# Optimization experiments

Hardware: AMD Instinct MI355X
Metric: run time of the kernel (lower is better)

The kernel has to match this reference:

```python
import jax, jax.numpy as jnp
import numpy as np
import math

RES = 1024          # FastTrigLookup / FastPhaseProcessor resolution
TWO_PI = 2.0 * math.pi
D = 512             # model dim


def setup_inputs() -> dict:
    key = jax.random.key(0)
    ks = jax.random.split(key, 4)
    B, L = 4, 4096

    def xavier(k, shape):
        fan_out, fan_in = shape
        std = math.sqrt(2.0 / (fan_in + fan_out))
        return jax.random.normal(k, shape, jnp.float32) * std

    return {
        "x": jax.random.normal(ks[0], (B, L, D), jnp.float32),
        "ft_w": xavier(ks[1], (2 * D, D)),
        "ft_b": jnp.zeros((2 * D,), jnp.float32),
        "ln_g": jnp.ones((2 * D,), jnp.float32),
        "ln_b": jnp.zeros((2 * D,), jnp.float32),
        "exc": jnp.ones((1,), jnp.float32) * 0.1,  # excitation_factor init
        "qkv_w": xavier(ks[2], (6 * D, 6 * D)),
        "qkv_b": jnp.zeros((6 * D,), jnp.float32),
        "op_w": xavier(ks[3], (2 * D, 2 * D)),
        "op_b": jnp.zeros((2 * D,), jnp.float32),
    }


def _forward(x, ft_w, ft_b, ln_g, ln_b, exc, qkv_w, qkv_b, op_w, op_b):
    B, L = x.shape[:2]
    sin_tab = jnp.sin(jnp.linspace(0.0, TWO_PI, RES)).astype(x.dtype)
    cos_tab = jnp.cos(jnp.linspace(0.0, TWO_PI, RES)).astype(x.dtype)

    # --- SimpleQuantumState: fused Linear -> tanh-GELU -> LayerNorm ---
    t = x @ ft_w.T + ft_b                                  # [B,L,2D]
    c1, c2 = 0.044715, math.sqrt(2.0 / math.pi)
    g = 0.5 * t * (1.0 + jnp.tanh(c2 * (t + c1 * t ** 3)))
    mu = g.mean(-1, keepdims=True)
    var = ((g - mu) ** 2).mean(-1, keepdims=True)
    n = (g - mu) * jax.lax.rsqrt(var + 1e-5) * ln_g + ln_b
    rp, ip = n[..., :D], n[..., D:]
    # atan2 -> gather-based sin/cos lookup (torch .long() truncates toward 0;
    # negative indices wrap from the end -> emulate with mod RES)
    ang = jnp.arctan2(ip + 1e-8, rp + 1e-8)
    idx = jnp.mod((ang / TWO_PI * (RES - 1)).astype(jnp.int32), RES)
    real = rp * cos_tab[idx]
    imag = ip * sin_tab[idx]
    nrm = jax.lax.rsqrt(real ** 2 + imag ** 2 + 1e-8) * math.sqrt(1.0 / D)
    real, imag = real * nrm, imag * nrm

    # --- EnhancedDynamicPhaseSpace: collapse prevention via trig lookup ---
    amp = jnp.sqrt(real ** 2 + imag ** 2 + 1e-8)
    coll = (amp < 0.1).astype(x.dtype)
    el = jnp.linspace(0.0, 1.0, D) * TWO_PI                # energy_levels * 2pi
    lidx = jnp.clip((jnp.mod(el, TWO_PI) / TWO_PI * RES).astype(jnp.int32), 0, RES - 1)
    real = real + coll * cos_tab[lidx] * exc
    imag = imag + coll * sin_tab[lidx] * exc
    nrm2 = jax.lax.rsqrt(real ** 2 + imag ** 2 + 1e-8)
    real, imag = real * nrm2, imag * nrm2

    # --- BasicQuantumAttention with q=k=v = quantum state (pad_mask=None) ---
    qkv_in = jnp.concatenate([real, imag, real, imag, real, imag], axis=-1)  # [B,L,6D]
    qkv = (qkv_in @ qkv_w.T + qkv_b).reshape(B, L, 6, D)
    q_r, k_r = qkv[:, :, 0], qkv[:, :, 2]
    v_r, v_i = qkv[:, :, 4], qkv[:, :, 5]
    scores = jnp.einsum('bld,bmd->blm', q_r, k_r) * (D ** -0.5)
    attn = jax.nn.softmax(scores, axis=-1)                 # dropout=eval -> identity
    o = jnp.concatenate([jnp.einsum('blm,bmd->bld', attn, v_r),
                         jnp.einsum('blm,bmd->bld', attn, v_i)], axis=-1)
    out = o @ op_w.T + op_b                                # [B,L,2D]
    return out


def reference(x, ft_w, ft_b, ln_g, ln_b, exc, qkv_w, qkv_b, op_w, op_b):
    out = _forward(x, ft_w, ft_b, ln_g, ln_b, exc, qkv_w, qkv_b, op_w, op_b)
    return (out[..., :D], out[..., D:])
```

## Files before the change

### kernel.cpp

```cpp
#include <hip/hip_runtime.h>
#include <hip/hip_bf16.h>
#include <math.h>


#define TWO_PI_F 6.283185307179586f

typedef __attribute__((ext_vector_type(4))) float f32x4;
typedef __attribute__((ext_vector_type(8))) short bf16x8;
typedef __attribute__((ext_vector_type(4))) unsigned short u16x4;
typedef __hip_bfloat16 bf16;

__device__ __forceinline__ void gl_lds16(const void* g, void* l) {
  __builtin_amdgcn_global_load_lds((const __attribute__((address_space(1))) void*)g,
                                   (__attribute__((address_space(3))) void*)l, 16, 0, 0);
}
__device__ __forceinline__ unsigned short f2bf_bits(float f) {
  union { __hip_bfloat16 h; unsigned short u; } cv;
  cv.h = __float2bfloat16(f);
  return cv.u;
}
__device__ __forceinline__ float bf_bits2f(unsigned short b) {
  union { unsigned int u; float f; } cv;
  cv.u = ((unsigned int)b) << 16;
  return cv.f;
}

template <int EPI, int ORD>
__global__ __launch_bounds__(256, 2) void gemm128(
    const bf16* __restrict__ A, const bf16* __restrict__ B, void* __restrict__ C,
    void* __restrict__ Cx, const float* __restrict__ bias, int K, int lda, int ldb, int ldc,
    float scale, long long zsa, long long zsb, long long zsc) {
  __shared__ __align__(16) bf16 sA[128 * 32];
  __shared__ __align__(16) bf16 sB[128 * 32];
  const int tid = threadIdx.x;
  const int lane = tid & 63, wid = tid >> 6;
  const int wm = wid >> 1, wn = wid & 1;

  const int gx = gridDim.x, gy = gridDim.y;
  int flat = blockIdx.x + gx * (blockIdx.y + gy * blockIdx.z);
  {
    const int nwg = gx * gy * gridDim.z;
    const int q = nwg >> 3, r = nwg & 7;
    const int x = flat & 7, loc = flat >> 3;
    flat = (x < r ? x * (q + 1) : r * (q + 1) + (x - r) * q) + loc;
  }
  const int bx = flat % gx;
  const int by = (flat / gx) % gy;
  const int bz = flat / (gx * gy);
  const int bm = by * 128, bn = bx * 128;

  const bf16* Az = A + (long long)bz * zsa;
  const bf16* Bz = B + (long long)bz * zsb;

  f32x4 acc[4][4];
#pragma unroll
  for (int i = 0; i < 4; ++i)
#pragma unroll
    for (int j = 0; j < 4; ++j) acc[i][j] = (f32x4){0.f, 0.f, 0.f, 0.f};

  const int r0 = tid >> 2, r1 = (tid + 256) >> 2, sl = tid & 3;
  const int swzr0 = (r0 & 3) ^ ((r0 >> 2) & 3);
  const int swzr1 = (r1 & 3) ^ ((r1 >> 2) & 3);
  const int ga0 = (sl ^ swzr0) << 3;
  const int ga1 = (sl ^ swzr1) << 3;
  const long long rowA0 = (long long)(bm + r0) * lda;
  const long long rowA1 = (long long)(bm + r1) * lda;
  const long long rowB0 = (long long)(bn + r0) * ldb;
  const long long rowB1 = (long long)(bn + r1) * ldb;

  const int fr = lane & 15, ksl = lane >> 4;

  for (int k0 = 0; k0 < K; k0 += 32) {
    gl_lds16(Az + rowA0 + k0 + ga0, &sA[tid * 8]);
    gl_lds16(Az + rowA1 + k0 + ga1, &sA[(tid + 256) * 8]);
    gl_lds16(Bz + rowB0 + k0 + ga0, &sB[tid * 8]);
    gl_lds16(Bz + rowB1 + k0 + ga1, &sB[(tid + 256) * 8]);
    __syncthreads();
    bf16x8 af[4], bfv[4];
#pragma unroll
    for (int i = 0; i < 4; ++i) {
      const int R = wm * 64 + i * 16 + fr;
      const int s = ksl ^ ((R & 3) ^ ((R >> 2) & 3));
      af[i] = *(const bf16x8*)&sA[R * 32 + s * 8];
    }
#pragma unroll
    for (int j = 0; j < 4; ++j) {
      const int R = wn * 64 + j * 16 + fr;
      const int s = ksl ^ ((R & 3) ^ ((R >> 2) & 3));
      bfv[j] = *(const bf16x8*)&sB[R * 32 + s * 8];
    }
#pragma unroll
    for (int i = 0; i < 4; ++i)
#pragma unroll
      for (int j = 0; j < 4; ++j) {
        if constexpr (ORD == 0)
          acc[i][j] = __builtin_amdgcn_mfma_f32_16x16x32_bf16(af[i], bfv[j], acc[i][j], 0, 0, 0);
        else
          acc[i][j] = __builtin_amdgcn_mfma_f32_16x16x32_bf16(bfv[j], af[i], acc[i][j], 0, 0, 0);
      }
    __syncthreads();
  }

#pragma unroll
  for (int i = 0; i < 4; ++i)
#pragma unroll
    for (int j = 0; j < 4; ++j) {
      if constexpr (ORD == 1) {
        const int row = bm + wm * 64 + i * 16 + fr;
        const int col0 = bn + wn * 64 + j * 16 + ksl * 4;
        f32x4 v = acc[i][j];
#pragma unroll
        for (int r = 0; r < 4; ++r) v[r] *= scale;
        if constexpr (EPI == 0 || EPI == 1) {
          if (bias) {
            const f32x4 bv = *(const f32x4*)&bias[col0];
            v += bv;
          }
        }
        if constexpr (EPI == 1) {
#pragma unroll
          for (int r = 0; r < 4; ++r) {
            const float t = v[r];
            float y = 0.7978845608028654f * (t + 0.044715f * t * t * t);
            y = fminf(fmaxf(y, -15.f), 15.f);
            const float e = __expf(2.f * y);
            v[r] = t * e / (1.f + e);
          }
        }
        if constexpr (EPI == 3) {
          const f32x4 bv = *(const f32x4*)&bias[col0];
          v += bv;
          float* dst = (col0 < 512) ? (float*)C : (float*)Cx;
          const long long rout = zsc + (long long)bz * 4096 + row;
          *(f32x4*)&dst[rout * 512 + (col0 & 511)] = v;
        } else if constexpr (EPI == 2) {
          bf16* cc = (bf16*)C + (long long)bz * zsc;
          u16x4 w;
#pragma unroll
          for (int r = 0; r < 4; ++r) w[r] = f2bf_bits(v[r]);
          *(u16x4*)&cc[(long long)row * ldc + col0] = w;
        } else {
          bf16* cc = (bf16*)C;
          u16x4 w;
#pragma unroll
          for (int r = 0; r < 4; ++r) w[r] = f2bf_bits(v[r]);
          *(u16x4*)&cc[(long long)row * ldc + col0] = w;
        }
      } else {
        const int row0 = bm + wm * 64 + i * 16 + ksl * 4;
        const int d = bn + wn * 64 + j * 16 + fr;
        u16x4 w;
#pragma unroll
        for (int r = 0; r < 4; ++r) w[r] = f2bf_bits(acc[i][j][r] * scale + bias[d]);
        const int b = row0 >> 12, mm = row0 & 4095;
        *(u16x4*)((unsigned short*)Cx + ((long long)(b * 1024 + d)) * 4096 + mm) = w;
      }
    }
  (void)ldc;
}

__global__ __launch_bounds__(256) void ln_phase_kernel(
    const bf16* __restrict__ g, bf16* __restrict__ u, const float* __restrict__ ln_g,
    const float* __restrict__ ln_b, const float* __restrict__ lcos,
    const float* __restrict__ lsin, const float* __restrict__ cost,
    const float* __restrict__ sint) {
  __shared__ float sg[1024];
  __shared__ float red[4];
  const int tid = threadIdx.x;
  const int lane = tid & 63, wid = tid >> 6;
  const long long row = blockIdx.x;
  const bf16* gr = g + row * 1024;

  const u16x4 raw = *(const u16x4*)(gr + tid * 4);
  float lv[4];
  float lsum = 0.f;
#pragma unroll
  for (int e = 0; e < 4; ++e) {
    lv[e] = bf_bits2f(raw[e]);
    lsum += lv[e];
  }
  *(f32x4*)&sg[tid * 4] = *(f32x4*)lv;
#pragma unroll
  for (int off = 32; off > 0; off >>= 1) lsum += __shfl_xor(lsum, off);
  if (lane == 0) red[wid] = lsum;
  __syncthreads();
  const float mu = (red[0] + red[1] + red[2] + red[3]) * (1.0f / 1024.0f);
  __syncthreads();
  float lvar = 0.f;
#pragma unroll
  for (int e = 0; e < 4; ++e) {
    const float d = lv[e] - mu;
    lvar += d * d;
  }
#pragma unroll
  for (int off = 32; off > 0; off >>= 1) lvar += __shfl_xor(lvar, off);
  if (lane == 0) red[wid] = lvar;
  __syncthreads();
  const float var = (red[0] + red[1] + red[2] + red[3]) * (1.0f / 1024.0f);
  const float rs = rsqrtf(var + 1e-5f);

#pragma unroll
  for (int kk = 0; kk < 2; ++kk) {
    const int p = tid + kk * 256;
    const float rp = (sg[p] - mu) * rs * ln_g[p] + ln_b[p];
    const float ip = (sg[p + 512] - mu) * rs * ln_g[p + 512] + ln_b[p + 512];
    const float ang = atan2f(ip + 1e-8f, rp + 1e-8f);
    int idx = (int)((ang / TWO_PI_F) * 1023.0f);
    idx = idx < 0 ? idx + 1024 : idx;
    float real = rp * cost[idx];
    float imag = ip * sint[idx];
    const float nrm = rsqrtf(real * real + imag * imag + 1e-8f) * 0.044194173824159216f;
    real *= nrm;
    imag *= nrm;
    const float amp = sqrtf(real * real + imag * imag + 1e-8f);
    const float coll = (amp < 0.1f) ? 1.0f : 0.0f;
    real += coll * lcos[p];
    imag += coll * lsin[p];
    const float n2 = rsqrtf(real * real + imag * imag + 1e-8f);
    u[row * 1024 + p] = __float2bfloat16(real * n2);
    u[row * 1024 + 512 + p] = __float2bfloat16(imag * n2);
  }
}

__global__ __launch_bounds__(256) void softmax_kernel(bf16* __restrict__ s) {
  __shared__ float ss[4096];
  __shared__ float red[4];
  const int tid = threadIdx.x;
  const int lane = tid & 63, wid = tid >> 6;
  bf16* sr = s + (long long)blockIdx.x * 4096;
  float mx = -3.0e38f;
#pragma unroll
  for (int k = 0; k < 4; ++k) {
    const int base = (k * 256 + tid) * 4;
    const u16x4 raw = *(const u16x4*)(sr + base);
    f32x4 f;
#pragma unroll
    for (int e = 0; e < 4; ++e) {
      f[e] = bf_bits2f(raw[e]);
      mx = fmaxf(mx, f[e]);
    }
    *(f32x4*)&ss[base] = f;
  }
#pragma unroll
  for (int off = 32; off > 0; off >>= 1) mx = fmaxf(mx, __shfl_xor(mx, off));
  if (lane == 0) red[wid] = mx;
  __syncthreads();
  mx = fmaxf(fmaxf(red[0], red[1]), fmaxf(red[2], red[3]));
  __syncthreads();
  float sum = 0.f;
#pragma unroll
  for (int k = 0; k < 4; ++k) {
    const int base = (k * 256 + tid) * 4;
    f32x4 f = *(f32x4*)&ss[base];
#pragma unroll
    for (int e = 0; e < 4; ++e) {
      f[e] = __expf(f[e] - mx);
      sum += f[e];
    }
    *(f32x4*)&ss[base] = f;
  }
#pragma unroll
  for (int off = 32; off > 0; off >>= 1) sum += __shfl_xor(sum, off);
  if (lane == 0) red[wid] = sum;
  __syncthreads();
  const float inv = 1.0f / (red[0] + red[1] + red[2] + red[3]);
#pragma unroll
  for (int k = 0; k < 4; ++k) {
    const int base = (k * 256 + tid) * 4;
    const f32x4 f = *(f32x4*)&ss[base];
    u16x4 w;
#pragma unroll
    for (int e = 0; e < 4; ++e) w[e] = f2bf_bits(f[e] * inv);
    *(u16x4*)(sr + base) = w;
  }
}

__global__ void cast4_f2b(const float* __restrict__ in, bf16* __restrict__ out, long long n4) {
  long long i = (long long)blockIdx.x * blockDim.x + threadIdx.x;
  const long long stride = (long long)gridDim.x * blockDim.x;
  for (; i < n4; i += stride) {
    const f32x4 f = *(const f32x4*)(in + i * 4);
    u16x4 w;
#pragma unroll
    for (int e = 0; e < 4; ++e) w[e] = f2bf_bits(f[e]);
    *(u16x4*)((unsigned short*)out + i * 4) = w;
  }
}

__global__ void fold_qkv(const float* __restrict__ w, const float* __restrict__ b,
                         bf16* __restrict__ weff, float* __restrict__ beff) {
  const int i = blockIdx.x * blockDim.x + threadIdx.x;
  if (i < 1024 * 1024) {
    const int o = i >> 10, j = i & 1023;
    const int so = (o < 512) ? o : o + 512;
    const float* wr = w + (long long)so * 3072;
    weff[i] = __float2bfloat16(wr[j] + wr[1024 + j] + wr[2048 + j]);
    if (j == 0) beff[o] = b[so];
  }
}

__global__ __launch_bounds__(256) void fold_v_t(const float* __restrict__ w,
                                                bf16* __restrict__ wvT) {
  __shared__ float tile[32][33];
  const int t0 = blockIdx.x * 32, j0 = blockIdx.y * 32;
  const int tx = threadIdx.x & 31, ty = threadIdx.x >> 5;
#pragma unroll
  for (int k = 0; k < 4; ++k) {
    const int t = t0 + ty + k * 8;
    const float* wr = w + (long long)(2048 + t) * 3072 + j0 + tx;
    tile[ty + k * 8][tx] = wr[0] + wr[1024] + wr[2048];
  }
  __syncthreads();
#pragma unroll
  for (int k = 0; k < 4; ++k) {
    const int r = ty + k * 8;
    wvT[(long long)(j0 + r) * 1024 + t0 + tx] = __float2bfloat16(tile[tx][r]);
  }
}

__global__ __launch_bounds__(256) void bias_fold2(const float* __restrict__ op_w,
                                                  const float* __restrict__ qkv_b,
                                                  float* __restrict__ beff) {
  __shared__ float red[4];
  const int o = blockIdx.x;
  const int tid = threadIdx.x, lane = tid & 63, wid = tid >> 6;
  float s = 0.f;
#pragma unroll
  for (int k = 0; k < 4; ++k) {
    const int t = tid + k * 256;
    s += op_w[(long long)o * 1024 + t] * qkv_b[2048 + t];
  }
#pragma unroll
  for (int off = 32; off > 0; off >>= 1) s += __shfl_xor(s, off);
  if (lane == 0) red[wid] = s;
  __syncthreads();
  if (tid == 0) beff[1024 + o] = red[0] + red[1] + red[2] + red[3];
}

__global__ void tables_kernel(float* __restrict__ cost, float* __restrict__ sint,
                              float* __restrict__ lcos, float* __restrict__ lsin,
                              const float* __restrict__ exc) {
  const int i = blockIdx.x * blockDim.x + threadIdx.x;
  const double step = 6.283185307179586 / 1023.0;
  if (i < 1024) {
    const float a = (float)((double)i * step);
    cost[i] = cosf(a);
    sint[i] = sinf(a);
  }
  if (i < 512) {
    const float el = ((float)i / 511.0f) * TWO_PI_F;
    const float m = fmodf(el, TWO_PI_F);
    int li = (int)((m / TWO_PI_F) * 1024.0f);
    li = min(max(li, 0), 1023);
    const float a = (float)((double)li * step);
    lcos[i] = cosf(a) * exc[0];
    lsin[i] = sinf(a) * exc[0];
  }
}

extern "C" void kernel_launch(void* const* d_in, const int* in_sizes, int n_in, void* d_out,
                              int out_size, void* d_ws, size_t ws_size, hipStream_t stream) {
  const float* x = (const float*)d_in[0];
  const float* ft_w = (const float*)d_in[1];
  const float* ft_b = (const float*)d_in[2];
  const float* ln_g = (const float*)d_in[3];
  const float* ln_b = (const float*)d_in[4];
  const float* exc = (const float*)d_in[5];
  const float* qkv_w = (const float*)d_in[6];
  const float* qkv_b = (const float*)d_in[7];
  const float* op_w = (const float*)d_in[8];
  const float* op_b = (const float*)d_in[9];

  char* ws = (char*)d_ws;
  const size_t MB = 1024ull * 1024ull;
  bf16* ftw_b = (bf16*)(ws + 0);
  bf16* weff = (bf16*)(ws + 1 * MB);
  bf16* opw_b = (bf16*)(ws + 5 * MB);
  bf16* wvT = (bf16*)(ws + 7 * MB);
  float* beff = (float*)(ws + 9 * MB);
  float* cost = (float*)(ws + 9 * MB + 8192);
  float* sint = (float*)(ws + 9 * MB + 12288);
  float* lcos = (float*)(ws + 9 * MB + 16384);
  float* lsin = (float*)(ws + 9 * MB + 18432);
  bf16* v2T = (bf16*)(ws + 10 * MB);
  bf16* qk = (bf16*)(ws + 42 * MB);
  bf16* x_b = (bf16*)(ws + 74 * MB);
  bf16* gbuf = (bf16*)(ws + 90 * MB);
  bf16* ubuf = (bf16*)(ws + 122 * MB);
  bf16* sc = (bf16*)(ws + 74 * MB);

  cast4_f2b<<<512, 256, 0, stream>>>(ft_w, ftw_b, 131072);
  cast4_f2b<<<1024, 256, 0, stream>>>(op_w, opw_b, 262144);
  cast4_f2b<<<2048, 256, 0, stream>>>(x, x_b, 2097152);
  fold_qkv<<<4096, 256, 0, stream>>>(qkv_w, qkv_b, weff, beff);
  fold_v_t<<<dim3(32, 32), 256, 0, stream>>>(qkv_w, wvT);
  bias_fold2<<<1024, 256, 0, stream>>>(op_w, qkv_b, beff);
  tables_kernel<<<4, 256, 0, stream>>>(cost, sint, lcos, lsin, exc);

  gemm128<0, 1><<<dim3(8, 8), 256, 0, stream>>>(opw_b, wvT, weff + 1024 * 1024, nullptr,
                                                nullptr, 1024, 1024, 1024, 1024, 1.0f, 0, 0, 0);
  gemm128<1, 1><<<dim3(8, 128), 256, 0, stream>>>(x_b, ftw_b, gbuf, nullptr, ft_b, 512, 512,
                                                  512, 1024, 1.0f, 0, 0, 0);
  ln_phase_kernel<<<16384, 256, 0, stream>>>(gbuf, ubuf, ln_g, ln_b, lcos, lsin, cost, sint);
  gemm128<0, 1><<<dim3(8, 128), 256, 0, stream>>>(ubuf, weff, qk, nullptr, beff, 1024, 1024,
                                                  1024, 1024, 1.0f, 0, 0, 0);
  gemm128<4, 0><<<dim3(8, 128), 256, 0, stream>>>(ubuf, weff + 1024 * 1024, nullptr, v2T,
                                                  beff + 1024, 1024, 1024, 1024, 0, 1.0f, 0,
                                                  0, 0);

  float* out0 = (float*)d_out;
  float* out1 = out0 + 8388608LL;
  for (int p = 0; p < 2; ++p) {
    const bf16* qbase = qk + (long long)(2 * p) * 4096 * 1024;
    gemm128<2, 1><<<dim3(32, 32, 2), 256, 0, stream>>>(
        qbase, qbase + 512, sc, nullptr, nullptr, 512, 1024, 1024, 4096,
        0.04419417382415922f, 4096LL * 1024, 4096LL * 1024, 4096LL * 4096);
    softmax_kernel<<<8192, 256, 0, stream>>>(sc);
    gemm128<3, 1><<<dim3(8, 32, 2), 256, 0, stream>>>(
        sc, v2T + (long long)(2 * p) * 1024 * 4096, out0, out1, op_b, 4096, 4096, 4096, 0,
        1.0f, 4096LL * 4096, 1024LL * 4096, (long long)(2 * p) * 4096);
  }
  (void)in_sizes;
  (void)n_in;
  (void)out_size;
  (void)ws_size;
}
```

Before: 525.8 us.

## Split-K the attention-value GEMM and merge the weight-folding prep kernels

Splits the K=4096 attn·V GEMM into two halves, doubling its grid from 512 to 1024 workgroups. The first half writes biased output directly and the second writes fp32 partials, which a new combine kernel adds into the output. Four small preprocessing kernels are also merged into one fold_all launch. This raises occupancy on the GEMM at the cost of 32MB of extra partial-buffer traffic and one extra launch per batch pair.

```diff
diff --git a/kernel.cpp b/kernel.cpp
--- a/kernel.cpp
+++ b/kernel.cpp
@@ -29,7 +29,8 @@
 __global__ __launch_bounds__(256, 2) void gemm128(
     const bf16* __restrict__ A, const bf16* __restrict__ B, void* __restrict__ C,
     void* __restrict__ Cx, const float* __restrict__ bias, int K, int lda, int ldb, int ldc,
-    float scale, long long zsa, long long zsb, long long zsc) {
+    float scale, long long zsa, long long zsb, long long zsc, float* __restrict__ P0,
+    float* __restrict__ P1) {
   __shared__ __align__(16) bf16 sA[128 * 32];
   __shared__ __align__(16) bf16 sB[128 * 32];
   const int tid = threadIdx.x;
@@ -49,8 +50,15 @@
   const int bz = flat / (gx * gy);
   const int bm = by * 128, bn = bx * 128;
 
-  const bf16* Az = A + (long long)bz * zsa;
-  const bf16* Bz = B + (long long)bz * zsb;
+  const bf16 *Az, *Bz;
+  if constexpr (EPI == 3) {
+    const int b = bz & 1, c = bz >> 1;
+    Az = A + (long long)b * zsa + c * 2048;
+    Bz = B + (long long)b * zsb + c * 2048;
+  } else {
+    Az = A + (long long)bz * zsa;
+    Bz = B + (long long)bz * zsb;
+  }
 
   f32x4 acc[4][4];
 #pragma unroll
@@ -128,11 +136,17 @@
           }
         }
         if constexpr (EPI == 3) {
-          const f32x4 bv = *(const f32x4*)&bias[col0];
-          v += bv;
-          float* dst = (col0 < 512) ? (float*)C : (float*)Cx;
-          const long long rout = zsc + (long long)bz * 4096 + row;
-          *(f32x4*)&dst[rout * 512 + (col0 & 511)] = v;
+          const int b = bz & 1, c = bz >> 1;
+          if (c == 0) {
+            const f32x4 bv = *(const f32x4*)&bias[col0];
+            v += bv;
+            float* dst = (col0 < 512) ? (float*)C : (float*)Cx;
+            const long long rout = zsc + (long long)b * 4096 + row;
+            *(f32x4*)&dst[rout * 512 + (col0 & 511)] = v;
+          } else {
+            float* dst = b ? P1 : P0;
+            *(f32x4*)&dst[(long long)row * 1024 + col0] = v;
+          }
         } else if constexpr (EPI == 2) {
           bf16* cc = (bf16*)C + (long long)bz * zsc;
           u16x4 w;
@@ -157,6 +171,24 @@
       }
     }
   (void)ldc;
+}
+
+__global__ __launch_bounds__(256) void combine_kernel(const float* __restrict__ p0,
+                                                      const float* __restrict__ p1,
+                                                      float* __restrict__ out0,
+                                                      float* __restrict__ out1) {
+  const int idx = blockIdx.x * 256 + threadIdx.x;
+  const int b = idx >> 20;
+  const int rem = idx & 1048575;
+  const int row = rem >> 8;
+  const int c4 = rem & 255;
+  const float* p = b ? p1 : p0;
+  const f32x4 v = *(const f32x4*)(p + (long long)row * 1024 + c4 * 4);
+  float* dst = (c4 < 128) ? out0 : out1;
+  const long long o = ((long long)(b * 4096 + row)) * 512 + (c4 & 127) * 4;
+  f32x4 d = *(f32x4*)(dst + o);
+  d += v;
+  *(f32x4*)(dst + o) = d;
 }
 
 __global__ __launch_bounds__(256) void ln_phase_kernel(
@@ -287,74 +319,72 @@
   }
 }
 
-__global__ void fold_qkv(const float* __restrict__ w, const float* __restrict__ b,
-                         bf16* __restrict__ weff, float* __restrict__ beff) {
-  const int i = blockIdx.x * blockDim.x + threadIdx.x;
-  if (i < 1024 * 1024) {
+__global__ __launch_bounds__(256) void fold_all(
+    const float* __restrict__ w, const float* __restrict__ b,
+    const float* __restrict__ op_w, const float* __restrict__ exc, bf16* __restrict__ weff,
+    bf16* __restrict__ wvT, float* __restrict__ beff, float* __restrict__ cost,
+    float* __restrict__ sint, float* __restrict__ lcos, float* __restrict__ lsin) {
+  __shared__ float tile[32][33];
+  __shared__ float red[4];
+  const int blk = blockIdx.x;
+  const int tid = threadIdx.x;
+  if (blk < 4096) {
+    const int i = blk * 256 + tid;
     const int o = i >> 10, j = i & 1023;
     const int so = (o < 512) ? o : o + 512;
     const float* wr = w + (long long)so * 3072;
     weff[i] = __float2bfloat16(wr[j] + wr[1024 + j] + wr[2048 + j]);
     if (j == 0) beff[o] = b[so];
-  }
-}
-
-__global__ __launch_bounds__(256) void fold_v_t(const float* __restrict__ w,
-                                                bf16* __restrict__ wvT) {
-  __shared__ float tile[32][33];
-  const int t0 = blockIdx.x * 32, j0 = blockIdx.y * 32;
-  const int tx = threadIdx.x & 31, ty = threadIdx.x >> 5;
-#pragma unroll
-  for (int k = 0; k < 4; ++k) {
-    const int t = t0 + ty + k * 8;
-    const float* wr = w + (long long)(2048 + t) * 3072 + j0 + tx;
-    tile[ty + k * 8][tx] = wr[0] + wr[1024] + wr[2048];
-  }
-  __syncthreads();
-#pragma unroll
-  for (int k = 0; k < 4; ++k) {
-    const int r = ty + k * 8;
-    wvT[(long long)(j0 + r) * 1024 + t0 + tx] = __float2bfloat16(tile[tx][r]);
-  }
-}
-
-__global__ __launch_bounds__(256) void bias_fold2(const float* __restrict__ op_w,
-                                                  const float* __restrict__ qkv_b,
-                                                  float* __restrict__ beff) {
-  __shared__ float red[4];
-  const int o = blockIdx.x;
-  const int tid = threadIdx.x, lane = tid & 63, wid = tid >> 6;
-  float s = 0.f;
-#pragma unroll
-  for (int k = 0; k < 4; ++k) {
-    const int t = tid + k * 256;
-    s += op_w[(long long)o * 1024 + t] * qkv_b[2048 + t];
-  }
-#pragma unroll
-  for (int off = 32; off > 0; off >>= 1) s += __shfl_xor(s, off);
-  if (lane == 0) red[wid] = s;
-  __syncthreads();
-  if (tid == 0) beff[1024 + o] = red[0] + red[1] + red[2] + red[3];
-}
-
-__global__ void tables_kernel(float* __restrict__ cost, float* __restrict__ sint,
-                              float* __restrict__ lcos, float* __restrict__ lsin,
-                              const float* __restrict__ exc) {
-  const int i = blockIdx.x * blockDim.x + threadIdx.x;
-  const double step = 6.283185307179586 / 1023.0;
-  if (i < 1024) {
-    const float a = (float)((double)i * step);
-    cost[i] = cosf(a);
-    sint[i] = sinf(a);
-  }
-  if (i < 512) {
-    const float el = ((float)i / 511.0f) * TWO_PI_F;
-    const float m = fmodf(el, TWO_PI_F);
-    int li = (int)((m / TWO_PI_F) * 1024.0f);
-    li = min(max(li, 0), 1023);
-    const float a = (float)((double)li * step);
-    lcos[i] = cosf(a) * exc[0];
-    lsin[i] = sinf(a) * exc[0];
+  } else if (blk < 5120) {
+    const int tb = blk - 4096;
+    const int t0 = (tb & 31) * 32, j0 = (tb >> 5) * 32;
+    const int tx = tid & 31, ty = tid >> 5;
+#pragma unroll
+    for (int k = 0; k < 4; ++k) {
+      const int t = t0 + ty + k * 8;
+      const float* wr = w + (long long)(2048 + t) * 3072 + j0 + tx;
+      tile[ty + k * 8][tx] = wr[0] + wr[1024] + wr[2048];
+    }
+    __syncthreads();
+#pragma unroll
+    for (int k = 0; k < 4; ++k) {
+      const int r = ty + k * 8;
+      wvT[(long long)(j0 + r) * 1024 + t0 + tx] = __float2bfloat16(tile[tx][r]);
+    }
+  } else if (blk < 6144) {
+    const int o = blk - 5120;
+    const int lane = tid & 63, wid = tid >> 6;
+    float s = 0.f;
+#pragma unroll
+    for (int k = 0; k < 4; ++k) {
+      const int t = tid + k * 256;
+      s += op_w[(long long)o * 1024 + t] * b[2048 + t];
+    }
+#pragma unroll
+    for (int off = 32; off > 0; off >>= 1) s += __shfl_xor(s, off);
+    if (lane == 0) red[wid] = s;
+    __syncthreads();
+    if (tid == 0) beff[1024 + o] = red[0] + red[1] + red[2] + red[3];
+  } else {
+    const double step = 6.283185307179586 / 1023.0;
+#pragma unroll
+    for (int k = 0; k < 4; ++k) {
+      const int i = tid + k * 256;
+      const float a = (float)((double)i * step);
+      cost[i] = cosf(a);
+      sint[i] = sinf(a);
+    }
+#pragma unroll
+    for (int k = 0; k < 2; ++k) {
+      const int i = tid + k * 256;
+      const float el = ((float)i / 511.0f) * TWO_PI_F;
+      const float m = fmodf(el, TWO_PI_F);
+      int li = (int)((m / TWO_PI_F) * 1024.0f);
+      li = min(max(li, 0), 1023);
+      const float a = (float)((double)li * step);
+      lcos[i] = cosf(a) * exc[0];
+      lsin[i] = sinf(a) * exc[0];
+    }
   }
 }
 
@@ -388,25 +418,26 @@
   bf16* gbuf = (bf16*)(ws + 90 * MB);
   bf16* ubuf = (bf16*)(ws + 122 * MB);
   bf16* sc = (bf16*)(ws + 74 * MB);
+  float* part0 = (float*)(ws + 138 * MB);
+  float* part1 = (float*)(ws + 154 * MB);
 
   cast4_f2b<<<512, 256, 0, stream>>>(ft_w, ftw_b, 131072);
   cast4_f2b<<<1024, 256, 0, stream>>>(op_w, opw_b, 262144);
   cast4_f2b<<<2048, 256, 0, stream>>>(x, x_b, 2097152);
-  fold_qkv<<<4096, 256, 0, stream>>>(qkv_w, qkv_b, weff, beff);
-  fold_v_t<<<dim3(32, 32), 256, 0, stream>>>(qkv_w, wvT);
-  bias_fold2<<<1024, 256, 0, stream>>>(op_w, qkv_b, beff);
-  tables_kernel<<<4, 256, 0, stream>>>(cost, sint, lcos, lsin, exc);
+  fold_all<<<6145, 256, 0, stream>>>(qkv_w, qkv_b, op_w, exc, weff, wvT, beff, cost, sint,
+                                     lcos, lsin);
 
   gemm128<0, 1><<<dim3(8, 8), 256, 0, stream>>>(opw_b, wvT, weff + 1024 * 1024, nullptr,
-                                                nullptr, 1024, 1024, 1024, 1024, 1.0f, 0, 0, 0);
+                                                nullptr, 1024, 1024, 1024, 1024, 1.0f, 0, 0,
+                                                0, nullptr, nullptr);
   gemm128<1, 1><<<dim3(8, 128), 256, 0, stream>>>(x_b, ftw_b, gbuf, nullptr, ft_b, 512, 512,
-                                                  512, 1024, 1.0f, 0, 0, 0);
+                                                  512, 1024, 1.0f, 0, 0, 0, nullptr, nullptr);
   ln_phase_kernel<<<16384, 256, 0, stream>>>(gbuf, ubuf, ln_g, ln_b, lcos, lsin, cost, sint);
   gemm128<0, 1><<<dim3(8, 128), 256, 0, stream>>>(ubuf, weff, qk, nullptr, beff, 1024, 1024,
-                                                  1024, 1024, 1.0f, 0, 0, 0);
+                                                  1024, 1024, 1.0f, 0, 0, 0, nullptr, nullptr);
   gemm128<4, 0><<<dim3(8, 128), 256, 0, stream>>>(ubuf, weff + 1024 * 1024, nullptr, v2T,
                                                   beff + 1024, 1024, 1024, 1024, 0, 1.0f, 0,
-                                                  0, 0);
+                                                  0, 0, nullptr, nullptr);
 
   float* out0 = (float*)d_out;
   float* out1 = out0 + 8388608LL;
@@ -414,11 +445,14 @@
     const bf16* qbase = qk + (long long)(2 * p) * 4096 * 1024;
     gemm128<2, 1><<<dim3(32, 32, 2), 256, 0, stream>>>(
         qbase, qbase + 512, sc, nullptr, nullptr, 512, 1024, 1024, 4096,
-        0.04419417382415922f, 4096LL * 1024, 4096LL * 1024, 4096LL * 4096);
+        0.04419417382415922f, 4096LL * 1024, 4096LL * 1024, 4096LL * 4096, nullptr, nullptr);
     softmax_kernel<<<8192, 256, 0, stream>>>(sc);
-    gemm128<3, 1><<<dim3(8, 32, 2), 256, 0, stream>>>(
-        sc, v2T + (long long)(2 * p) * 1024 * 4096, out0, out1, op_b, 4096, 4096, 4096, 0,
-        1.0f, 4096LL * 4096, 1024LL * 4096, (long long)(2 * p) * 4096);
+    gemm128<3, 1><<<dim3(8, 32, 4), 256, 0, stream>>>(
+        sc, v2T + (long long)(2 * p) * 1024 * 4096, out0, out1, op_b, 2048, 4096, 4096, 0,
+        1.0f, 4096LL * 4096, 1024LL * 4096, (long long)(2 * p) * 4096, part0, part1);
+    combine_kernel<<<8192, 256, 0, stream>>>(part0, part1,
+                                             out0 + (long long)(2 * p) * 4096 * 512,
+                                             out1 + (long long)(2 * p) * 4096 * 512);
   }
   (void)in_sizes;
   (void)n_in;
```

Result: no change. 535.4 us (+1.8%).
